# Kernel optimization log

Measured on AMD Instinct MI355X. Metric: run time of the kernel, lower is better.

The kernel has to match this reference:

```python
import jax, jax.numpy as jnp
import numpy as np

N_HEADS = 16
LN_EPS = 1e-5


def setup_inputs() -> dict:
    key = jax.random.key(0)
    ks = jax.random.split(key, 7)
    B, N, DIN, DCOND, NF = 2, 512, 1024, 128, 8
    return {
        "x": jax.random.normal(ks[0], (B, N, DIN), jnp.float32),
        "code": jax.random.normal(ks[1], (DCOND, NF), jnp.float32),
        "w_c": jax.random.normal(ks[2], (DIN, DCOND), jnp.float32) * 0.02,
        "W": jax.random.normal(ks[3], (3 * DIN, DIN), jnp.float32) * 0.02,
        "b": jax.random.normal(ks[4], (3 * DIN,), jnp.float32) * 0.02,
        "gamma": jnp.ones((DIN,), jnp.float32),
        "beta": jnp.zeros((DIN,), jnp.float32),
    }


def _layernorm(h, gamma, beta):
    mu = jnp.mean(h, axis=-1, keepdims=True)
    var = jnp.var(h, axis=-1, keepdims=True)
    return (h - mu) * jax.lax.rsqrt(var + LN_EPS) * gamma + beta


def reference(x, code, w_c, W, b, gamma, beta):
    B, N, din = x.shape
    nf = code.shape[1]
    H = N_HEADS
    hd = din // H
    scale = hd ** (-0.5)

    # ModLin2D: condition codes -> (nf, din), layernormed
    cond = _layernorm((w_c @ code).T, gamma, beta)            # (nf, din)
    # FiLM-style broadcasted multiply: (B, nf, N, din)
    modx = x[:, None, :, :] * cond[None, :, None, :]
    # projection to qkv: (B, nf, N, 3*din)
    qkv = jnp.einsum('bfnd,ed->bfne', modx, W) + b

    # split channel dim as (3, H, hd); torch view(3,H,hd,B,nf,N) on
    # channel-first layout == reshape (..., 3, H, hd) here
    qkv = qkv.reshape(B, nf, N, 3, H, hd)
    qkv = jnp.transpose(qkv, (3, 0, 4, 1, 2, 5))              # (3, B, H, nf, N, hd)
    q, k = qkv[0], qkv[1]

    scores = jnp.einsum('bhfnd,bhfmd->bhfnm', q, k) * scale   # (B, H, nf, N, N)
    attn = jax.nn.softmax(scores, axis=-1)
    # original torch code returns attn.size(); we return attn (the computed tensor)
    return attn
```

## Files before the change

### kernel.cpp

```cpp
#include <hip/hip_runtime.h>
#include <hip/hip_bf16.h>
#include <math.h>

#define NB    2
#define NSEQ  512
#define DIN   1024
#define DCOND 128
#define NF    8
#define NH    16
#define HD    64
constexpr float LN_EPS = 1e-5f;

#define WS_COND 0
#define WS_AHI  32768
#define WS_ALO  16809984
#define WS_BHI  33587200
#define WS_BLO  37781504
#define WS_QB   41975808
#define WS_KB   75530240

using bf16x8 = __attribute__((ext_vector_type(8))) short;
using f32x4  = __attribute__((ext_vector_type(4))) float;

__device__ __forceinline__ unsigned short f2bf(float x) {
    unsigned int u = __float_as_uint(x);
    unsigned int r = (u + 0x7fffu + ((u >> 16) & 1u)) >> 16;
    return (unsigned short)r;
}
__device__ __forceinline__ float bf2f(unsigned short h) {
    return __uint_as_float(((unsigned int)h) << 16);
}

__device__ __forceinline__ void gload16(const void* g, void* l) {
    __builtin_amdgcn_global_load_lds(
        (__attribute__((address_space(1))) void*)(const_cast<void*>(g)),
        (__attribute__((address_space(3))) void*)l, 16, 0, 0);
}

__global__ __launch_bounds__(256)
void cond_kernel(const float* __restrict__ w_c, const float* __restrict__ code,
                 const float* __restrict__ gamma, const float* __restrict__ beta,
                 float* __restrict__ cond)
{
    __shared__ float sc[DCOND];
    __shared__ float rs[256], rs2[256];
    const int f = blockIdx.x;
    const int t = threadIdx.x;

    if (t < DCOND) sc[t] = code[t * NF + f];
    __syncthreads();

    float hv[4];
    float s = 0.f, s2 = 0.f;
#pragma unroll
    for (int r = 0; r < 4; ++r) {
        const int d = r * 256 + t;
        const float* row = w_c + (size_t)d * DCOND;
        float acc = 0.f;
#pragma unroll 8
        for (int c = 0; c < DCOND; c += 4) {
            float4 wv = *(const float4*)(row + c);
            float4 cv = *(const float4*)(sc + c);
            acc += wv.x * cv.x + wv.y * cv.y + wv.z * cv.z + wv.w * cv.w;
        }
        hv[r] = acc; s += acc; s2 += acc * acc;
    }
    rs[t] = s; rs2[t] = s2;
    __syncthreads();
    for (int off = 128; off > 0; off >>= 1) {
        if (t < off) { rs[t] += rs[t + off]; rs2[t] += rs2[t + off]; }
        __syncthreads();
    }
    const float mu  = rs[0] * (1.f / DIN);
    const float var = rs2[0] * (1.f / DIN) - mu * mu;
    const float rstd = rsqrtf(var + LN_EPS);
#pragma unroll
    for (int r = 0; r < 4; ++r) {
        const int d = r * 256 + t;
        cond[f * DIN + d] = (hv[r] - mu) * rstd * gamma[d] + beta[d];
    }
}

__global__ __launch_bounds__(256)
void split_x_kernel(const float* __restrict__ x, const float* __restrict__ cond,
                    short* __restrict__ Ahi, short* __restrict__ Alo)
{
    const unsigned idx = blockIdx.x * 256 + threadIdx.x;
    const int d  = (idx & 127) * 8;
    const int n  = (idx >> 7) & 511;
    const int bf = idx >> 16;
    const int b  = bf >> 3, f = bf & 7;

    const float* xs = x + ((size_t)b * NSEQ + n) * DIN + d;
    const float* cs = cond + f * DIN + d;
    float4 x0 = *(const float4*)xs,      x1 = *(const float4*)(xs + 4);
    float4 c0 = *(const float4*)cs,      c1 = *(const float4*)(cs + 4);

    float m[8] = { x0.x*c0.x, x0.y*c0.y, x0.z*c0.z, x0.w*c0.w,
                   x1.x*c1.x, x1.y*c1.y, x1.z*c1.z, x1.w*c1.w };
    bf16x8 hi, lo;
#pragma unroll
    for (int i = 0; i < 8; ++i) {
        unsigned short h = f2bf(m[i]);
        hi[i] = (short)h;
        lo[i] = (short)f2bf(m[i] - bf2f(h));
    }
    *(bf16x8*)(Ahi + (size_t)idx * 8) = hi;
    *(bf16x8*)(Alo + (size_t)idx * 8) = lo;
}

__global__ __launch_bounds__(256)
void split_w_kernel(const float* __restrict__ W,
                    short* __restrict__ Bhi, short* __restrict__ Blo)
{
    const unsigned idx = blockIdx.x * 256 + threadIdx.x;
    const float* ws = W + (size_t)idx * 8;
    float4 w0 = *(const float4*)ws, w1 = *(const float4*)(ws + 4);
    float m[8] = { w0.x, w0.y, w0.z, w0.w, w1.x, w1.y, w1.z, w1.w };
    bf16x8 hi, lo;
#pragma unroll
    for (int i = 0; i < 8; ++i) {
        unsigned short h = f2bf(m[i]);
        hi[i] = (short)h;
        lo[i] = (short)f2bf(m[i] - bf2f(h));
    }
    *(bf16x8*)(Bhi + (size_t)idx * 8) = hi;
    *(bf16x8*)(Blo + (size_t)idx * 8) = lo;
}

__global__ __launch_bounds__(256, 2)
void proj_mfma_kernel(const short* __restrict__ Ahi_g, const short* __restrict__ Alo_g,
                      const short* __restrict__ Bhi_g, const short* __restrict__ Blo_g,
                      const float* __restrict__ bias,
                      float* __restrict__ Qb, float* __restrict__ Kb)
{
    __shared__ short sAhi[128 * 32];
    __shared__ short sAlo[128 * 32];
    __shared__ short sBhi[128 * 32];
    __shared__ short sBlo[128 * 32];

    const int bf   = blockIdx.z;
    const int n0   = blockIdx.y * 128;
    const int bcol = blockIdx.x * 128;
    const int t    = threadIdx.x;
    const int w    = t >> 6, lane = t & 63;
    const int wr   = w >> 1, wc = w & 1;

    const int rl = lane >> 2;
    const int sl = (lane & 3) ^ ((lane >> 3) & 3);
    const size_t aoff = ((size_t)bf * NSEQ + n0 + 32 * w + rl) * DIN + sl * 8;
    const size_t boff = ((size_t)(bcol + 32 * w + rl)) * DIN + sl * 8;
    const short* gAh = Ahi_g + aoff;
    const short* gAl = Alo_g + aoff;
    const short* gBh = Bhi_g + boff;
    const short* gBl = Blo_g + boff;
    short* dAh = sAhi + 1024 * w;
    short* dAl = sAlo + 1024 * w;
    short* dBh = sBhi + 1024 * w;
    short* dBl = sBlo + 1024 * w;

    int offA[4], offB[4];
    const int g = lane >> 4;
#pragma unroll
    for (int fi = 0; fi < 4; ++fi) {
        int r  = wr * 64 + fi * 16 + (lane & 15);
        offA[fi] = r * 32 + ((g ^ ((r >> 1) & 3)) * 8);
        int rb = wc * 64 + fi * 16 + (lane & 15);
        offB[fi] = rb * 32 + ((g ^ ((rb >> 1) & 3)) * 8);
    }

    f32x4 acc[4][4];
#pragma unroll
    for (int i = 0; i < 4; ++i)
#pragma unroll
        for (int j = 0; j < 4; ++j) acc[i][j] = (f32x4){0.f, 0.f, 0.f, 0.f};

    for (int kb = 0; kb < DIN; kb += 32) {
        __syncthreads();
        gload16(gAh + kb, dAh);  gload16(gAh + kb + 16 * DIN, dAh + 512);
        gload16(gAl + kb, dAl);  gload16(gAl + kb + 16 * DIN, dAl + 512);
        gload16(gBh + kb, dBh);  gload16(gBh + kb + 16 * DIN, dBh + 512);
        gload16(gBl + kb, dBl);  gload16(gBl + kb + 16 * DIN, dBl + 512);
        __syncthreads();

        bf16x8 Ah[4], Al[4], Bh[4], Bl[4];
#pragma unroll
        for (int fi = 0; fi < 4; ++fi) {
            Ah[fi] = *(const bf16x8*)(sAhi + offA[fi]);
            Al[fi] = *(const bf16x8*)(sAlo + offA[fi]);
            Bh[fi] = *(const bf16x8*)(sBhi + offB[fi]);
            Bl[fi] = *(const bf16x8*)(sBlo + offB[fi]);
        }
#pragma unroll
        for (int i = 0; i < 4; ++i)
#pragma unroll
            for (int j = 0; j < 4; ++j) {
                acc[i][j] = __builtin_amdgcn_mfma_f32_16x16x32_bf16(Ah[i], Bh[j], acc[i][j], 0, 0, 0);
                acc[i][j] = __builtin_amdgcn_mfma_f32_16x16x32_bf16(Ah[i], Bl[j], acc[i][j], 0, 0, 0);
                acc[i][j] = __builtin_amdgcn_mfma_f32_16x16x32_bf16(Al[i], Bh[j], acc[i][j], 0, 0, 0);
            }
    }

#pragma unroll
    for (int j = 0; j < 4; ++j) {
        const int e = bcol + wc * 64 + j * 16 + (lane & 15);
        const float bv = bias[e];
        const int ek = e & 1023;
        float* dst = ((e < DIN) ? Qb : Kb)
                   + ((size_t)(bf * NH + (ek >> 6)) * NSEQ) * HD + (ek & 63);
#pragma unroll
        for (int i = 0; i < 4; ++i) {
            const int rbase = n0 + wr * 64 + i * 16 + (lane >> 4) * 4;
            f32x4 v = acc[i][j];
#pragma unroll
            for (int rg = 0; rg < 4; ++rg)
                dst[(size_t)(rbase + rg) * HD] = v[rg] + bv;
        }
    }
}

__global__ __launch_bounds__(256, 2)
void scores_smx_kernel(const float* __restrict__ Qb, const float* __restrict__ Kb,
                       float* __restrict__ out)
{
    constexpr int LQ = 68;
    __shared__ float Qs[HD][LQ];
    __shared__ float Ks[HD][LQ];

    const int bfh = blockIdx.y;
    const int rt  = blockIdx.x;
    const int t = threadIdx.x, tx = t & 15, ty = t >> 4;

    const float* Qp = Qb + ((size_t)bfh * NSEQ + rt * 64) * HD;
    const float* Kp = Kb + (size_t)bfh * NSEQ * HD;

    const int b = bfh >> 7, f = (bfh >> 4) & 7, h = bfh & 15;
    const size_t obase = ((((size_t)(b * NH + h)) * NF + f) * NSEQ + rt * 64) * NSEQ;

    const int li = t >> 2, lg0 = t & 3;

#pragma unroll
    for (int gg = 0; gg < 4; ++gg) {
        const int gq = lg0 + gg * 4;
        float4 v = *(const float4*)(Qp + (size_t)li * HD + gq * 4);
        Qs[gq * 4 + 0][li] = v.x; Qs[gq * 4 + 1][li] = v.y;
        Qs[gq * 4 + 2][li] = v.z; Qs[gq * 4 + 3][li] = v.w;
    }

    float acc[8][4][4];
#pragma unroll
    for (int ct = 0; ct < 8; ++ct)
#pragma unroll
        for (int i = 0; i < 4; ++i)
#pragma unroll
            for (int j = 0; j < 4; ++j) acc[ct][i][j] = 0.f;

#pragma unroll
    for (int ct = 0; ct < 8; ++ct) {
        __syncthreads();
#pragma unroll
        for (int gg = 0; gg < 4; ++gg) {
            const int gq = lg0 + gg * 4;
            float4 v = *(const float4*)(Kp + (size_t)(ct * 64 + li) * HD + gq * 4);
            Ks[gq * 4 + 0][li] = v.x; Ks[gq * 4 + 1][li] = v.y;
            Ks[gq * 4 + 2][li] = v.z; Ks[gq * 4 + 3][li] = v.w;
        }
        __syncthreads();
#pragma unroll 4
        for (int d = 0; d < HD; ++d) {
            float4 a = *(const float4*)&Qs[d][ty * 4];
            float4 bb = *(const float4*)&Ks[d][tx * 4];
            float av[4] = {a.x, a.y, a.z, a.w};
            float bv[4] = {bb.x, bb.y, bb.z, bb.w};
#pragma unroll
            for (int i = 0; i < 4; ++i)
#pragma unroll
                for (int j = 0; j < 4; ++j)
                    acc[ct][i][j] += av[i] * bv[j];
        }
    }

#pragma unroll
    for (int i = 0; i < 4; ++i) {
        float m = -1e30f;
#pragma unroll
        for (int ct = 0; ct < 8; ++ct)
#pragma unroll
            for (int j = 0; j < 4; ++j) m = fmaxf(m, acc[ct][i][j]);
        m = fmaxf(m, __shfl_xor(m, 1));
        m = fmaxf(m, __shfl_xor(m, 2));
        m = fmaxf(m, __shfl_xor(m, 4));
        m = fmaxf(m, __shfl_xor(m, 8));

        float s = 0.f;
#pragma unroll
        for (int ct = 0; ct < 8; ++ct)
#pragma unroll
            for (int j = 0; j < 4; ++j) {
                float e = __expf((acc[ct][i][j] - m) * 0.125f);
                acc[ct][i][j] = e;
                s += e;
            }
        s += __shfl_xor(s, 1);
        s += __shfl_xor(s, 2);
        s += __shfl_xor(s, 4);
        s += __shfl_xor(s, 8);
        const float inv = 1.f / s;

        const size_t rowoff = obase + (size_t)(ty * 4 + i) * NSEQ;
#pragma unroll
        for (int ct = 0; ct < 8; ++ct) {
            float4 v = make_float4(acc[ct][i][0] * inv, acc[ct][i][1] * inv,
                                   acc[ct][i][2] * inv, acc[ct][i][3] * inv);
            *(float4*)(out + rowoff + ct * 64 + tx * 4) = v;
        }
    }
}

extern "C" void kernel_launch(void* const* d_in, const int* in_sizes, int n_in,
                              void* d_out, int out_size, void* d_ws, size_t ws_size,
                              hipStream_t stream)
{
    const float* x     = (const float*)d_in[0];
    const float* code  = (const float*)d_in[1];
    const float* w_c   = (const float*)d_in[2];
    const float* W     = (const float*)d_in[3];
    const float* bias  = (const float*)d_in[4];
    const float* gamma = (const float*)d_in[5];
    const float* beta  = (const float*)d_in[6];
    float* out = (float*)d_out;

    char* ws = (char*)d_ws;
    float* cond = (float*)(ws + WS_COND);
    short* Ahi  = (short*)(ws + WS_AHI);
    short* Alo  = (short*)(ws + WS_ALO);
    short* Bhi  = (short*)(ws + WS_BHI);
    short* Blo  = (short*)(ws + WS_BLO);
    float* Qb   = (float*)(ws + WS_QB);
    float* Kb   = (float*)(ws + WS_KB);

    cond_kernel<<<NF, 256, 0, stream>>>(w_c, code, gamma, beta, cond);
    split_x_kernel<<<4096, 256, 0, stream>>>(x, cond, Ahi, Alo);
    split_w_kernel<<<1024, 256, 0, stream>>>(W, Bhi, Blo);

    dim3 gP(16, 4, NB * NF);
    proj_mfma_kernel<<<gP, 256, 0, stream>>>(Ahi, Alo, Bhi, Blo, bias, Qb, Kb);

    dim3 gS(8, NB * NF * NH);
    scores_smx_kernel<<<gS, 256, 0, stream>>>(Qb, Kb, out);
}
```

Baseline: 524.1 us.

## Compute attention scores with split-bf16 MFMA and swizzled async K staging

Replaces the scalar FP32 QK^T scores kernel with one that splits Q and K into bf16 hi/lo pairs and runs three MFMA 16x16x32 products per tile to approximate FP32 accuracy. K tiles are loaded directly into LDS with global_load_lds using an XOR swizzle to avoid bank conflicts. Each wave now owns whole score rows, so the softmax reduction uses only cross-group shuffles. It gives up some precision through truncation-based splitting and the dropped lo*lo term, and it holds 128 accumulator registers per lane.

```diff
diff --git a/kernel.cpp b/kernel.cpp
--- a/kernel.cpp
+++ b/kernel.cpp
@@ -35,6 +35,21 @@
     __builtin_amdgcn_global_load_lds(
         (__attribute__((address_space(1))) void*)(const_cast<void*>(g)),
         (__attribute__((address_space(3))) void*)l, 16, 0, 0);
+}
+
+struct BF2 { bf16x8 hi, lo; };
+__device__ __forceinline__ BF2 split8(float4 a, float4 b) {
+    float v[8] = {a.x, a.y, a.z, a.w, b.x, b.y, b.z, b.w};
+    BF2 r;
+#pragma unroll
+    for (int i = 0; i < 8; ++i) {
+        unsigned u  = __float_as_uint(v[i]);
+        unsigned uh = u & 0xffff0000u;
+        r.hi[i] = (short)(u >> 16);
+        float l = v[i] - __uint_as_float(uh);
+        r.lo[i] = (short)(__float_as_uint(l) >> 16);
+    }
+    return r;
 }
 
 __global__ __launch_bounds__(256)
@@ -93,8 +108,8 @@
 
     const float* xs = x + ((size_t)b * NSEQ + n) * DIN + d;
     const float* cs = cond + f * DIN + d;
-    float4 x0 = *(const float4*)xs,      x1 = *(const float4*)(xs + 4);
-    float4 c0 = *(const float4*)cs,      c1 = *(const float4*)(cs + 4);
+    float4 x0 = *(const float4*)xs, x1 = *(const float4*)(xs + 4);
+    float4 c0 = *(const float4*)cs, c1 = *(const float4*)(cs + 4);
 
     float m[8] = { x0.x*c0.x, x0.y*c0.y, x0.z*c0.z, x0.w*c0.w,
                    x1.x*c1.x, x1.y*c1.y, x1.z*c1.z, x1.w*c1.w };
@@ -220,100 +235,91 @@
 }
 
 __global__ __launch_bounds__(256, 2)
-void scores_smx_kernel(const float* __restrict__ Qb, const float* __restrict__ Kb,
-                       float* __restrict__ out)
-{
-    constexpr int LQ = 68;
-    __shared__ float Qs[HD][LQ];
-    __shared__ float Ks[HD][LQ];
+void scores_mfma_kernel(const float* __restrict__ Qb, const float* __restrict__ Kb,
+                        float* __restrict__ out)
+{
+    __shared__ float Kl_lds[128 * 64];
 
     const int bfh = blockIdx.y;
     const int rt  = blockIdx.x;
-    const int t = threadIdx.x, tx = t & 15, ty = t >> 4;
-
-    const float* Qp = Qb + ((size_t)bfh * NSEQ + rt * 64) * HD;
+    const int t = threadIdx.x, w = t >> 6, lane = t & 63;
+    const int g = lane >> 4, c16 = lane & 15;
+
+    const float* Qp = Qb + ((size_t)bfh * NSEQ + rt * 64 + 16 * w + c16) * HD;
+    BF2 qf[2];
+#pragma unroll
+    for (int ks = 0; ks < 2; ++ks) {
+        float4 a = *(const float4*)(Qp + 32 * ks + 8 * g);
+        float4 b = *(const float4*)(Qp + 32 * ks + 8 * g + 4);
+        qf[ks] = split8(a, b);
+    }
+
     const float* Kp = Kb + (size_t)bfh * NSEQ * HD;
+    const int swz = (lane & 7) << 4;
+
+    f32x4 acc[32];
+#pragma unroll
+    for (int i = 0; i < 32; ++i) acc[i] = (f32x4){0.f, 0.f, 0.f, 0.f};
+
+#pragma unroll
+    for (int c = 0; c < 4; ++c) {
+        __syncthreads();
+#pragma unroll
+        for (int i = 0; i < 8; ++i) {
+            const int row = 32 * w + 4 * i + g;
+            const int slot = c16 ^ (row & 7);
+            gload16(Kp + ((size_t)(c * 128 + row)) * HD + slot * 4,
+                    Kl_lds + (32 * w + 4 * i) * HD);
+        }
+        __syncthreads();
+
+#pragma unroll
+        for (int mtl = 0; mtl < 8; ++mtl) {
+            const int row = 16 * mtl + c16;
+            const char* rbase = (const char*)Kl_lds + row * 256;
+#pragma unroll
+            for (int ks = 0; ks < 2; ++ks) {
+                const int o = 128 * ks + 32 * g;
+                float4 a = *(const float4*)(rbase + ((o)      ^ swz));
+                float4 b = *(const float4*)(rbase + ((o + 16) ^ swz));
+                BF2 kf = split8(a, b);
+                f32x4 d = acc[c * 8 + mtl];
+                d = __builtin_amdgcn_mfma_f32_16x16x32_bf16(kf.hi, qf[ks].hi, d, 0, 0, 0);
+                d = __builtin_amdgcn_mfma_f32_16x16x32_bf16(kf.hi, qf[ks].lo, d, 0, 0, 0);
+                d = __builtin_amdgcn_mfma_f32_16x16x32_bf16(kf.lo, qf[ks].hi, d, 0, 0, 0);
+                acc[c * 8 + mtl] = d;
+            }
+        }
+    }
+
+    float m = -1e30f;
+#pragma unroll
+    for (int i = 0; i < 32; ++i)
+#pragma unroll
+        for (int r = 0; r < 4; ++r) m = fmaxf(m, acc[i][r]);
+    m = fmaxf(m, __shfl_xor(m, 16));
+    m = fmaxf(m, __shfl_xor(m, 32));
+
+    float s = 0.f;
+#pragma unroll
+    for (int i = 0; i < 32; ++i)
+#pragma unroll
+        for (int r = 0; r < 4; ++r) {
+            float e = __expf((acc[i][r] - m) * 0.125f);
+            acc[i][r] = e;
+            s += e;
+        }
+    s += __shfl_xor(s, 16);
+    s += __shfl_xor(s, 32);
+    const float inv = 1.f / s;
 
     const int b = bfh >> 7, f = (bfh >> 4) & 7, h = bfh & 15;
-    const size_t obase = ((((size_t)(b * NH + h)) * NF + f) * NSEQ + rt * 64) * NSEQ;
-
-    const int li = t >> 2, lg0 = t & 3;
-
-#pragma unroll
-    for (int gg = 0; gg < 4; ++gg) {
-        const int gq = lg0 + gg * 4;
-        float4 v = *(const float4*)(Qp + (size_t)li * HD + gq * 4);
-        Qs[gq * 4 + 0][li] = v.x; Qs[gq * 4 + 1][li] = v.y;
-        Qs[gq * 4 + 2][li] = v.z; Qs[gq * 4 + 3][li] = v.w;
-    }
-
-    float acc[8][4][4];
-#pragma unroll
-    for (int ct = 0; ct < 8; ++ct)
-#pragma unroll
-        for (int i = 0; i < 4; ++i)
-#pragma unroll
-            for (int j = 0; j < 4; ++j) acc[ct][i][j] = 0.f;
-
-#pragma unroll
-    for (int ct = 0; ct < 8; ++ct) {
-        __syncthreads();
-#pragma unroll
-        for (int gg = 0; gg < 4; ++gg) {
-            const int gq = lg0 + gg * 4;
-            float4 v = *(const float4*)(Kp + (size_t)(ct * 64 + li) * HD + gq * 4);
-            Ks[gq * 4 + 0][li] = v.x; Ks[gq * 4 + 1][li] = v.y;
-            Ks[gq * 4 + 2][li] = v.z; Ks[gq * 4 + 3][li] = v.w;
-        }
-        __syncthreads();
-#pragma unroll 4
-        for (int d = 0; d < HD; ++d) {
-            float4 a = *(const float4*)&Qs[d][ty * 4];
-            float4 bb = *(const float4*)&Ks[d][tx * 4];
-            float av[4] = {a.x, a.y, a.z, a.w};
-            float bv[4] = {bb.x, bb.y, bb.z, bb.w};
-#pragma unroll
-            for (int i = 0; i < 4; ++i)
-#pragma unroll
-                for (int j = 0; j < 4; ++j)
-                    acc[ct][i][j] += av[i] * bv[j];
-        }
-    }
-
-#pragma unroll
-    for (int i = 0; i < 4; ++i) {
-        float m = -1e30f;
-#pragma unroll
-        for (int ct = 0; ct < 8; ++ct)
-#pragma unroll
-            for (int j = 0; j < 4; ++j) m = fmaxf(m, acc[ct][i][j]);
-        m = fmaxf(m, __shfl_xor(m, 1));
-        m = fmaxf(m, __shfl_xor(m, 2));
-        m = fmaxf(m, __shfl_xor(m, 4));
-        m = fmaxf(m, __shfl_xor(m, 8));
-
-        float s = 0.f;
-#pragma unroll
-        for (int ct = 0; ct < 8; ++ct)
-#pragma unroll
-            for (int j = 0; j < 4; ++j) {
-                float e = __expf((acc[ct][i][j] - m) * 0.125f);
-                acc[ct][i][j] = e;
-                s += e;
-            }
-        s += __shfl_xor(s, 1);
-        s += __shfl_xor(s, 2);
-        s += __shfl_xor(s, 4);
-        s += __shfl_xor(s, 8);
-        const float inv = 1.f / s;
-
-        const size_t rowoff = obase + (size_t)(ty * 4 + i) * NSEQ;
-#pragma unroll
-        for (int ct = 0; ct < 8; ++ct) {
-            float4 v = make_float4(acc[ct][i][0] * inv, acc[ct][i][1] * inv,
-                                   acc[ct][i][2] * inv, acc[ct][i][3] * inv);
-            *(float4*)(out + rowoff + ct * 64 + tx * 4) = v;
-        }
+    const int n = rt * 64 + 16 * w + c16;
+    float* rowp = out + ((((size_t)(b * NH + h)) * NF + f) * NSEQ + n) * NSEQ;
+#pragma unroll
+    for (int i = 0; i < 32; ++i) {
+        f32x4 v = acc[i] * inv;
+        *(f32x4*)(rowp + 16 * i + 4 * g) = v;
     }
 }
 
@@ -347,5 +353,5 @@
     proj_mfma_kernel<<<gP, 256, 0, stream>>>(Ahi, Alo, Bhi, Blo, bias, Qb, Kb);
 
     dim3 gS(8, NB * NF * NH);
-    scores_smx_kernel<<<gS, 256, 0, stream>>>(Qb, Kb, out);
-}
+    scores_mfma_kernel<<<gS, 256, 0, stream>>>(Qb, Kb, out);
+}
```

After: 469.7 us. -10.4%, faster.
